# Performance work log

Hardware: AMD Instinct MI355X
Metric: run time of the kernel (lower is better)

Reference implementation:

```python
import jax, jax.numpy as jnp
import numpy as np

B, T, F_IN, N, H = 16, 2048, 64, 24, 64  # batch, time, input_dim, num_nodes, hidden_dim
ALPHA = 0.2        # LeakyReLU negative slope
NEG_INF = -9e15    # mask value used by the torch module


def setup_inputs() -> dict:
    key = jax.random.key(0)
    k0, k1, k2, k3, k4 = jax.random.split(key, 5)
    x = jax.random.normal(k0, (B, T, F_IN), dtype=jnp.float32)
    adj = jax.random.randint(k1, (N, N), 0, 2, dtype=jnp.int32)  # binary adjacency
    # input_projector: Linear(input_dim, num_nodes*hidden_dim)
    Wp = jax.random.normal(k2, (F_IN, N * H), dtype=jnp.float32) * 0.05
    bp = jnp.zeros((N * H,), dtype=jnp.float32)
    # GraphAttentionLayer params: W (in=H, out=H), a (2H, 1)
    W = jax.random.normal(k3, (H, H), dtype=jnp.float32) * 0.05
    a = jax.random.normal(k4, (2 * H, 1), dtype=jnp.float32) * 0.05
    return {"x": x, "adj": adj, "Wp": Wp, "bp": bp, "W": W, "a": a}


def reference(x, adj, Wp, bp, W, a):
    Bx, Tx, Fx = x.shape
    BT = Bx * Tx
    # input projector -> per-node features (BT, N, H)
    h = (x.reshape(BT, Fx) @ Wp + bp).reshape(BT, N, H)
    # GAT layer (concat=True), eval mode so dropout is identity
    Wh = h @ W  # (BT, N, H)
    # e[b,i,j] = LeakyReLU([Wh_i ; Wh_j] @ a) = LeakyReLU(Wh_i@a1 + Wh_j@a2)
    a1, a2 = a[:H, 0], a[H:, 0]
    f1 = Wh @ a1  # (BT, N)
    f2 = Wh @ a2  # (BT, N)
    e = f1[:, :, None] + f2[:, None, :]
    e = jnp.where(e > 0, e, ALPHA * e)
    e = jnp.where(adj[None, :, :] > 0, e, jnp.float32(NEG_INF))
    attn = jax.nn.softmax(e, axis=2)  # (BT, N, N)
    h_prime = jnp.einsum('bij,bjh->bih', attn, Wh)  # (BT, N, H)
    h_prime = jax.nn.elu(h_prime)
    out = h_prime.mean(axis=1)  # mean over nodes -> (BT, H)
    return out.reshape(Bx, Tx, H)
```

## Files before the change

kernel.cpp:

```cpp
#include <hip/hip_runtime.h>
#include <hip/hip_bf16.h>

#define F_IN   64
#define NN     24
#define HH     64
#define CC     1536
#define CCX    1584
#define NTILE  99
#define ROWS   16
#define BT_TOT (16 * 2048)
#define ALPHA_ 0.2f
#define NEG_INF_ -9.0e15f
#define LOG2E_ 1.4426950408889634f
#define XSP    72
#define ATS    24

typedef short bf16x8 __attribute__((ext_vector_type(8)));
typedef float f32x4  __attribute__((ext_vector_type(4)));

#if defined(__has_builtin)
#  if __has_builtin(__builtin_amdgcn_cvt_pk_bf16_f32)
#    define HAS_PK_BF16 1
#  endif
#  if __has_builtin(__builtin_amdgcn_exp2f)
#    define HAS_EXP2 1
#  endif
#endif
#ifndef HAS_PK_BF16
#  define HAS_PK_BF16 0
#endif
#ifndef HAS_EXP2
#  define HAS_EXP2 0
#endif

__device__ __forceinline__ short f2bf(float f) {
    unsigned u = __float_as_uint(f);
    return (short)((u + 0x7FFFu + ((u >> 16) & 1u)) >> 16);
}

__device__ __forceinline__ int pk2bf(float a, float b) {
#if HAS_PK_BF16
    typedef __bf16 bfv2 __attribute__((ext_vector_type(2)));
    bfv2 r = __builtin_amdgcn_cvt_pk_bf16_f32(a, b);
    return __builtin_bit_cast(int, r);
#else
    return (int)(unsigned short)f2bf(a) | ((int)f2bf(b) << 16);
#endif
}

__device__ __forceinline__ float exp2_fast(float x) {
#if HAS_EXP2
    return __builtin_amdgcn_exp2f(x);
#else
    return __expf(0.6931471805599453f * x);
#endif
}

__global__ __launch_bounds__(256) void precompute_kernel(
    const float* __restrict__ Wp,
    const float* __restrict__ bp,
    const float* __restrict__ W,
    const float* __restrict__ a,
    const int*   __restrict__ adj,
    short* __restrict__ Bpk,
    float* __restrict__ bpWx,
    float* __restrict__ maskf)
{
    __shared__ float WpS[64 * 65];
    __shared__ float WS[64 * 17];
    __shared__ float Wa[128];
    const int b = blockIdx.x, tid = threadIdx.x;

    if (b < 96) {
        const int n64 = (b >> 2) * 64;
        const int jc0 = (b & 3) * 16;
        for (int i = tid; i < 4096; i += 256)
            WpS[(i >> 6) * 65 + (i & 63)] = Wp[(size_t)(i >> 6) * CC + n64 + (i & 63)];
        for (int i = tid; i < 1024; i += 256)
            WS[(i >> 4) * 17 + (i & 15)] = W[(i >> 4) * 64 + jc0 + (i & 15)];
        __syncthreads();

        const int k = tid & 63, q0 = (tid >> 6) * 4;
        float acc[4] = {0.f, 0.f, 0.f, 0.f};
        #pragma unroll 4
        for (int m = 0; m < 64; ++m) {
            const float wp = WpS[k * 65 + m];
            #pragma unroll
            for (int j = 0; j < 4; ++j)
                acc[j] += wp * WS[m * 17 + q0 + j];
        }
        const int s2 = k >> 5, jj = k & 7, lbase = ((k >> 3) & 3) * 16;
        #pragma unroll
        for (int j = 0; j < 4; ++j) {
            const int l = lbase + q0 + j;
            Bpk[((size_t)(b * 2 + s2) * 64 + l) * 8 + jj] = f2bf(acc[j]);
        }
    } else {
        const bool needWa = (b < 108) || (b == 114);
        if (needWa) {
            if (tid < 128) {
                const int which = tid >> 6, m = tid & 63;
                float s = 0.f;
                #pragma unroll 8
                for (int h = 0; h < 64; ++h)
                    s += W[m * 64 + h] * a[which * 64 + h];
                Wa[tid] = s;
            }
            __syncthreads();
        }
        if (b < 108) {
            const int u  = (b - 96) * 256 + tid;
            const int jj = u & 7, l = (u >> 3) & 63, s2 = (u >> 9) & 1, te = u >> 10;
            const int t  = 96 + te;
            const int k  = s2 * 32 + ((l >> 4) << 3) + jj;
            const int ff = te * 16 + (l & 15);
            const int which = (ff >= NN) ? 1 : 0;
            const int node  = ff - which * NN;
            float v = 0.f;
            #pragma unroll 8
            for (int m = 0; m < 64; ++m)
                v += Wp[(size_t)k * CC + node * 64 + m] * Wa[which * 64 + m];
            Bpk[((size_t)(t * 2 + s2) * 64 + l) * 8 + jj] = f2bf(v * LOG2E_);
        } else {
            const int c = (b - 108) * 256 + tid;
            if (c < CC) {
                const int n = c >> 6, jc = c & 63;
                float s = 0.f;
                #pragma unroll 8
                for (int m = 0; m < 64; ++m) s += bp[n * 64 + m] * W[m * 64 + jc];
                bpWx[c] = s;
            } else if (c < CCX) {
                const int ff = c - CC;
                const int which = (ff >= NN) ? 1 : 0;
                const int node  = ff - which * NN;
                float s = 0.f;
                #pragma unroll 8
                for (int m = 0; m < 64; ++m) s += bp[node * 64 + m] * Wa[which * 64 + m];
                bpWx[c] = s * LOG2E_;
            }
            if (b == 114) {
                for (int i = tid; i < NN * NN; i += 256)
                    maskf[i] = (adj[i] > 0) ? 0.f : NEG_INF_;
            }
        }
    }
}

__global__ __launch_bounds__(1024, 8) void gat_main_kernel(
    const float* __restrict__ x,
    const float* __restrict__ maskf,
    const short* __restrict__ Bpk,
    const float* __restrict__ bpWx,
    float* __restrict__ out)
{
    __shared__ __align__(16) short xs16[ROWS * XSP];
    __shared__ __align__(16) short whB[ROWS * 4 * 48 * 8];
    __shared__ __align__(16) short attn16[ROWS * NN * ATS];
    __shared__ __align__(16) short zero16[8];
    __shared__ __align__(16) float maskS[NN * NN];
    __shared__ float fs[ROWS * 48];

    const int tid  = threadIdx.x;
    const int lane = tid & 63;
    const int wid  = tid >> 6;
    const int quad = lane >> 4;
    const int lm   = lane & 15;
    const size_t base = (size_t)blockIdx.x * ROWS;

    if (tid < 8) zero16[tid] = 0;
    if (tid < NN * NN) maskS[tid] = maskf[tid];
    {
        const int rr = tid >> 6, k = tid & 63;
        xs16[rr * XSP + k] = f2bf(x[base * F_IN + tid]);
    }
    __syncthreads();

    {
        const bf16x8 a0 = *(const bf16x8*)(xs16 + lm * XSP + quad * 8);
        const bf16x8 a1 = *(const bf16x8*)(xs16 + lm * XSP + 32 + quad * 8);

        auto tile_step = [&](int t) {
            const short* bq = Bpk + ((size_t)(t * 2) * 64 + lane) * 8;
            const bf16x8 b0 = *(const bf16x8*)bq;
            const bf16x8 b1 = *(const bf16x8*)(bq + 512);
            const float bb = bpWx[t * 16 + lm];
            f32x4 acc = {bb, bb, bb, bb};
            acc = __builtin_amdgcn_mfma_f32_16x16x32_bf16(a0, b0, acc, 0, 0, 0);
            acc = __builtin_amdgcn_mfma_f32_16x16x32_bf16(a1, b1, acc, 0, 0, 0);
            if (t < 96) {
                const int node = t >> 2, nt = t & 3;
                const int bi = (nt * 48 + (node >> 3) * 16 + lm) * 8 + (node & 7);
                const int p01 = pk2bf(acc[0], acc[1]);
                const int p23 = pk2bf(acc[2], acc[3]);
                short* wb = whB + quad * 4 * 1536 + bi;
                wb[0]        = (short)p01;
                wb[1536]     = (short)(p01 >> 16);
                wb[2 * 1536] = (short)p23;
                wb[3 * 1536] = (short)(p23 >> 16);
            } else {
                const int ff = (t - 96) * 16 + lm;
                #pragma unroll
                for (int i = 0; i < 4; ++i)
                    fs[(quad * 4 + i) * 48 + ff] = acc[i];
            }
        };

        #pragma unroll 3
        for (int tt = 0; tt < 6; ++tt)
            tile_step(wid * 6 + tt);
        if (wid < 3)
            tile_step(96 + wid);
    }
    __syncthreads();

    const int r = wid;
    short* attn_r = attn16 + r * NN * ATS;

    const float fval = (lane < 2 * NN) ? fs[r * 48 + lane] : 0.f;

    const int mr = (lane < NN) ? lane : 0;
    float mrow[NN];
    #pragma unroll
    for (int q = 0; q < 6; ++q)
        *(float4*)(mrow + 4 * q) = *(const float4*)(maskS + mr * NN + 4 * q);

    float ev[NN];
    float ssum = 0.f;
    const float f1i = fval;
    #pragma unroll
    for (int j = 0; j < NN; ++j) {
        float f2j = __shfl(fval, NN + j, 64);
        float e = f1i + f2j;
        e = fmaxf(e, ALPHA_ * e);
        ev[j] = exp2_fast(e + mrow[j]);
        ssum += ev[j];
    }
    const float inv = 1.f / ssum;
    if (lane < NN) {
        #pragma unroll
        for (int q = 0; q < 3; ++q) {
            int4 pq;
            pq.x = pk2bf(ev[8 * q]     * inv, ev[8 * q + 1] * inv);
            pq.y = pk2bf(ev[8 * q + 2] * inv, ev[8 * q + 3] * inv);
            pq.z = pk2bf(ev[8 * q + 4] * inv, ev[8 * q + 5] * inv);
            pq.w = pk2bf(ev[8 * q + 6] * inv, ev[8 * q + 7] * inv);
            *(int4*)(attn_r + lane * ATS + 8 * q) = pq;
        }
    }

    const short* pa0src = (quad < 3) ? (attn_r + lm * ATS + quad * 8) : zero16;
    const short* pa1src = (quad < 3 && lm < 8)
        ? (attn_r + (16 + lm) * ATS + quad * 8) : zero16;
    const bf16x8 pa0 = *(const bf16x8*)pa0src;
    const bf16x8 pa1 = *(const bf16x8*)pa1src;
    #pragma unroll
    for (int nt = 0; nt < 4; ++nt) {
        const short* bsrc = (lane < 48)
            ? (whB + r * 1536 + (nt * 48 + lane) * 8) : zero16;
        const bf16x8 bw = *(const bf16x8*)bsrc;
        f32x4 c0 = {0.f, 0.f, 0.f, 0.f};
        f32x4 c1 = {0.f, 0.f, 0.f, 0.f};
        c0 = __builtin_amdgcn_mfma_f32_16x16x32_bf16(pa0, bw, c0, 0, 0, 0);
        c1 = __builtin_amdgcn_mfma_f32_16x16x32_bf16(pa1, bw, c1, 0, 0, 0);
        float s = 0.f;
        #pragma unroll
        for (int i = 0; i < 4; ++i) {
            const float v = c0[i];
            s += (v > 0.f) ? v : (__expf(v) - 1.f);
        }
        #pragma unroll
        for (int i = 0; i < 4; ++i) {
            const float v = c1[i];
            s += (v > 0.f) ? v : (__expf(v) - 1.f);
        }
        s += __shfl_xor(s, 16, 64);
        s += __shfl_xor(s, 32, 64);
        if (quad == 0)
            out[(base + r) * HH + nt * 16 + lm] = s * (1.0f / 24.0f);
    }
}

extern "C" void kernel_launch(void* const* d_in, const int* in_sizes, int n_in,
                              void* d_out, int out_size, void* d_ws, size_t ws_size,
                              hipStream_t stream)
{
    const float* x   = (const float*)d_in[0];
    const int*   adj = (const int*)d_in[1];
    const float* Wp  = (const float*)d_in[2];
    const float* bp  = (const float*)d_in[3];
    const float* W   = (const float*)d_in[4];
    const float* a   = (const float*)d_in[5];
    float* out = (float*)d_out;

    short* Bpk   = (short*)d_ws;
    float* bpWx  = (float*)(Bpk + (size_t)NTILE * 1024);
    float* maskf = bpWx + CCX;

    precompute_kernel<<<115, 256, 0, stream>>>(Wp, bp, W, a, adj, Bpk, bpWx, maskf);
    gat_main_kernel<<<BT_TOT / ROWS, 1024, 0, stream>>>(x, maskf, Bpk, bpWx, out);
}
```

Baseline: 117.1 us.

## Repartition projection tiles per wave and split softmax rows across half-waves

The projection stage now gives each of 12 waves one node group and one hidden tile, so four node tiles are computed together and their bf16 results are packed into wider int2 stores instead of scattered 16-bit stores. Three further waves handle the attention-logit tiles. The softmax now splits each row's 24 columns across two half-waves of 12, loading f2 and mask values as vectors instead of shuffling them in, combining the partial sums with a single xor shuffle and using a hardware reciprocal. This cuts per-lane serial exp work and LDS store count, but leaves waves 12-15 idle or lightly loaded in the projection stage.

Measured after the change: 111.9 us. 1.05x faster.

```diff
diff --git a/kernel.cpp b/kernel.cpp
--- a/kernel.cpp
+++ b/kernel.cpp
@@ -25,12 +25,18 @@
 #  if __has_builtin(__builtin_amdgcn_exp2f)
 #    define HAS_EXP2 1
 #  endif
+#  if __has_builtin(__builtin_amdgcn_rcpf)
+#    define HAS_RCP 1
+#  endif
 #endif
 #ifndef HAS_PK_BF16
 #  define HAS_PK_BF16 0
 #endif
 #ifndef HAS_EXP2
 #  define HAS_EXP2 0
+#endif
+#ifndef HAS_RCP
+#  define HAS_RCP 0
 #endif
 
 __device__ __forceinline__ short f2bf(float f) {
@@ -53,6 +59,14 @@
     return __builtin_amdgcn_exp2f(x);
 #else
     return __expf(0.6931471805599453f * x);
+#endif
+}
+
+__device__ __forceinline__ float rcp_fast(float x) {
+#if HAS_RCP
+    return __builtin_amdgcn_rcpf(x);
+#else
+    return 1.0f / x;
 #endif
 }
 
@@ -179,7 +193,35 @@
         const bf16x8 a0 = *(const bf16x8*)(xs16 + lm * XSP + quad * 8);
         const bf16x8 a1 = *(const bf16x8*)(xs16 + lm * XSP + 32 + quad * 8);
 
-        auto tile_step = [&](int t) {
+        if (wid < 12) {
+            const int g  = wid >> 2;
+            const int nt = wid & 3;
+            short* wb0 = whB + ((nt * 48 + g * 16 + lm) * 8) + quad * 4 * 1536;
+            #pragma unroll 1
+            for (int half = 0; half < 2; ++half) {
+                f32x4 acc[4];
+                #pragma unroll
+                for (int k = 0; k < 4; ++k) {
+                    const int t = (g * 8 + half * 4 + k) * 4 + nt;
+                    const short* bq = Bpk + ((size_t)(t * 2) * 64 + lane) * 8;
+                    const bf16x8 b0 = *(const bf16x8*)bq;
+                    const bf16x8 b1 = *(const bf16x8*)(bq + 512);
+                    const float bb = bpWx[t * 16 + lm];
+                    f32x4 c = {bb, bb, bb, bb};
+                    c = __builtin_amdgcn_mfma_f32_16x16x32_bf16(a0, b0, c, 0, 0, 0);
+                    c = __builtin_amdgcn_mfma_f32_16x16x32_bf16(a1, b1, c, 0, 0, 0);
+                    acc[k] = c;
+                }
+                #pragma unroll
+                for (int i = 0; i < 4; ++i) {
+                    int2 w;
+                    w.x = pk2bf(acc[0][i], acc[1][i]);
+                    w.y = pk2bf(acc[2][i], acc[3][i]);
+                    *(int2*)(wb0 + i * 1536 + half * 4) = w;
+                }
+            }
+        } else if (wid < 15) {
+            const int t = 96 + (wid - 12);
             const short* bq = Bpk + ((size_t)(t * 2) * 64 + lane) * 8;
             const bf16x8 b0 = *(const bf16x8*)bq;
             const bf16x8 b1 = *(const bf16x8*)(bq + 512);
@@ -187,64 +229,67 @@
             f32x4 acc = {bb, bb, bb, bb};
             acc = __builtin_amdgcn_mfma_f32_16x16x32_bf16(a0, b0, acc, 0, 0, 0);
             acc = __builtin_amdgcn_mfma_f32_16x16x32_bf16(a1, b1, acc, 0, 0, 0);
-            if (t < 96) {
-                const int node = t >> 2, nt = t & 3;
-                const int bi = (nt * 48 + (node >> 3) * 16 + lm) * 8 + (node & 7);
-                const int p01 = pk2bf(acc[0], acc[1]);
-                const int p23 = pk2bf(acc[2], acc[3]);
-                short* wb = whB + quad * 4 * 1536 + bi;
-                wb[0]        = (short)p01;
-                wb[1536]     = (short)(p01 >> 16);
-                wb[2 * 1536] = (short)p23;
-                wb[3 * 1536] = (short)(p23 >> 16);
-            } else {
-                const int ff = (t - 96) * 16 + lm;
-                #pragma unroll
-                for (int i = 0; i < 4; ++i)
-                    fs[(quad * 4 + i) * 48 + ff] = acc[i];
-            }
-        };
-
-        #pragma unroll 3
-        for (int tt = 0; tt < 6; ++tt)
-            tile_step(wid * 6 + tt);
-        if (wid < 3)
-            tile_step(96 + wid);
+            const int ff = (t - 96) * 16 + lm;
+            #pragma unroll
+            for (int i = 0; i < 4; ++i)
+                fs[(quad * 4 + i) * 48 + ff] = acc[i];
+        }
     }
     __syncthreads();
 
     const int r = wid;
     short* attn_r = attn16 + r * NN * ATS;
 
-    const float fval = (lane < 2 * NN) ? fs[r * 48 + lane] : 0.f;
-
-    const int mr = (lane < NN) ? lane : 0;
-    float mrow[NN];
+    const int g  = lane >> 5;
+    const int i  = lane & 31;
+    const int jb = g * 12;
+
+    const float f1i = fs[r * 48 + i];
+    const int mr = (i < NN) ? i : 0;
+
+    float f2v[12], mrow[12];
+    {
+        const float* fp = fs + r * 48 + NN + jb;
+        const float4 fa = *(const float4*)(fp);
+        const float4 fb = *(const float4*)(fp + 4);
+        const float4 fc = *(const float4*)(fp + 8);
+        f2v[0]=fa.x; f2v[1]=fa.y; f2v[2]=fa.z; f2v[3]=fa.w;
+        f2v[4]=fb.x; f2v[5]=fb.y; f2v[6]=fb.z; f2v[7]=fb.w;
+        f2v[8]=fc.x; f2v[9]=fc.y; f2v[10]=fc.z; f2v[11]=fc.w;
+        const float* mp = maskS + mr * NN + jb;
+        const float4 ma = *(const float4*)(mp);
+        const float4 mb = *(const float4*)(mp + 4);
+        const float4 mc = *(const float4*)(mp + 8);
+        mrow[0]=ma.x; mrow[1]=ma.y; mrow[2]=ma.z; mrow[3]=ma.w;
+        mrow[4]=mb.x; mrow[5]=mb.y; mrow[6]=mb.z; mrow[7]=mb.w;
+        mrow[8]=mc.x; mrow[9]=mc.y; mrow[10]=mc.z; mrow[11]=mc.w;
+    }
+
+    float ev[12];
+    float ssum = 0.f;
     #pragma unroll
-    for (int q = 0; q < 6; ++q)
-        *(float4*)(mrow + 4 * q) = *(const float4*)(maskS + mr * NN + 4 * q);
-
-    float ev[NN];
-    float ssum = 0.f;
-    const float f1i = fval;
-    #pragma unroll
-    for (int j = 0; j < NN; ++j) {
-        float f2j = __shfl(fval, NN + j, 64);
-        float e = f1i + f2j;
+    for (int j = 0; j < 12; ++j) {
+        float e = f1i + f2v[j];
         e = fmaxf(e, ALPHA_ * e);
-        ev[j] = exp2_fast(e + mrow[j]);
-        ssum += ev[j];
-    }
-    const float inv = 1.f / ssum;
-    if (lane < NN) {
+        const float p = exp2_fast(e + mrow[j]);
+        ev[j] = p;
+        ssum += p;
+    }
+    const float tot = ssum + __shfl_xor(ssum, 32, 64);
+    const float inv = rcp_fast(tot);
+
+    if (i < NN) {
+        int pq[6];
         #pragma unroll
-        for (int q = 0; q < 3; ++q) {
-            int4 pq;
-            pq.x = pk2bf(ev[8 * q]     * inv, ev[8 * q + 1] * inv);
-            pq.y = pk2bf(ev[8 * q + 2] * inv, ev[8 * q + 3] * inv);
-            pq.z = pk2bf(ev[8 * q + 4] * inv, ev[8 * q + 5] * inv);
-            pq.w = pk2bf(ev[8 * q + 6] * inv, ev[8 * q + 7] * inv);
-            *(int4*)(attn_r + lane * ATS + 8 * q) = pq;
+        for (int q = 0; q < 6; ++q)
+            pq[q] = pk2bf(ev[2 * q] * inv, ev[2 * q + 1] * inv);
+        short* dst = attn_r + i * ATS + jb;
+        if (g == 0) {
+            *(int4*)(dst)     = make_int4(pq[0], pq[1], pq[2], pq[3]);
+            *(int2*)(dst + 8) = make_int2(pq[4], pq[5]);
+        } else {
+            *(int2*)(dst)     = make_int2(pq[0], pq[1]);
+            *(int4*)(dst + 4) = make_int4(pq[2], pq[3], pq[4], pq[5]);
         }
     }
 
@@ -264,13 +309,13 @@
         c1 = __builtin_amdgcn_mfma_f32_16x16x32_bf16(pa1, bw, c1, 0, 0, 0);
         float s = 0.f;
         #pragma unroll
-        for (int i = 0; i < 4; ++i) {
-            const float v = c0[i];
+        for (int k = 0; k < 4; ++k) {
+            const float v = c0[k];
             s += (v > 0.f) ? v : (__expf(v) - 1.f);
         }
         #pragma unroll
-        for (int i = 0; i < 4; ++i) {
-            const float v = c1[i];
+        for (int k = 0; k < 4; ++k) {
+            const float v = c1[k];
             s += (v > 0.f) ? v : (__expf(v) - 1.f);
         }
         s += __shfl_xor(s, 16, 64);
```
